# Performance work log

Hardware: AMD Instinct MI355X
Metric: run time of the kernel (lower is better)

## Reference

```python
import jax, jax.numpy as jnp
import numpy as np

N, E, G = 40000, 400000, 64
IN, ED, HID, HEADS, OUT = 2, 18, 64, 4, 3

def _glorot(key, shape):
    fan_in = shape[0]
    return jax.random.normal(key, shape, dtype=jnp.float32) / np.float32(np.sqrt(fan_in))

def setup_inputs():
    key = jax.random.key(0)
    ks = jax.random.split(key, 32)
    d1 = HEADS * HID  # 256
    return {
        "x": jax.random.normal(ks[0], (N, IN), jnp.float32),
        "edge_index": jax.random.randint(ks[1], (2, E), 0, N),
        "edge_attr": jax.random.normal(ks[2], (E, ED), jnp.float32),
        "batch": jnp.sort(jax.random.randint(ks[3], (N,), 0, G)),
        # conv1: TransformerConv(2 -> 64, heads=4, concat=True, beta=True, edge_dim=18)
        "Wq1": _glorot(ks[4], (IN, d1)), "bq1": jnp.zeros((d1,), jnp.float32),
        "Wk1": _glorot(ks[5], (IN, d1)), "bk1": jnp.zeros((d1,), jnp.float32),
        "Wv1": _glorot(ks[6], (IN, d1)), "bv1": jnp.zeros((d1,), jnp.float32),
        "We1": _glorot(ks[7], (ED, d1)),
        "Wskip1": _glorot(ks[8], (IN, d1)), "bskip1": jnp.zeros((d1,), jnp.float32),
        "Wbeta1": _glorot(ks[9], (3 * d1, 1)),
        # conv2: TransformerConv(256 -> 64, heads=1, concat=False, beta=True, edge_dim=18)
        "Wq2": _glorot(ks[10], (d1, HID)), "bq2": jnp.zeros((HID,), jnp.float32),
        "Wk2": _glorot(ks[11], (d1, HID)), "bk2": jnp.zeros((HID,), jnp.float32),
        "Wv2": _glorot(ks[12], (d1, HID)), "bv2": jnp.zeros((HID,), jnp.float32),
        "We2": _glorot(ks[13], (ED, HID)),
        "Wskip2": _glorot(ks[14], (d1, HID)), "bskip2": jnp.zeros((HID,), jnp.float32),
        "Wbeta2": _glorot(ks[15], (3 * HID, 1)),
        "Wlin": _glorot(ks[16], (HID, OUT)), "blin": jnp.zeros((OUT,), jnp.float32),
    }

def _tconv(x, src, dst, edge_attr, Wq, bq, Wk, bk, Wv, bv, We, Wskip, bskip, Wbeta, H, C, concat):
    # PyG TransformerConv with edge_dim, beta=True, root_weight=True (eval: dropout off)
    n = x.shape[0]
    q = (x @ Wq + bq).reshape(n, H, C)
    k = (x @ Wk + bk).reshape(n, H, C)
    v = (x @ Wv + bv).reshape(n, H, C)
    e = (edge_attr @ We).reshape(-1, H, C)              # [E,H,C]
    kj = k[src] + e                                      # key_j + edge
    alpha = jnp.einsum('ehc,ehc->eh', q[dst], kj) * (1.0 / (C ** 0.5))  # [E,H]
    # segment softmax over destination nodes
    amax = jax.ops.segment_max(alpha, dst, num_segments=n)
    ex = jnp.exp(alpha - amax[dst])
    den = jax.ops.segment_sum(ex, dst, num_segments=n)
    w = ex / (den[dst] + 1e-16)
    msg = (v[src] + e) * w[:, :, None]                   # [E,H,C]
    out = jax.ops.segment_sum(msg, dst, num_segments=n)  # [N,H,C]
    out = out.reshape(n, H * C) if concat else out.mean(axis=1)
    # beta-gated skip connection
    xr = x @ Wskip + bskip
    beta = jax.nn.sigmoid(jnp.concatenate([out, xr, out - xr], axis=-1) @ Wbeta)
    return beta * xr + (1.0 - beta) * out

def reference(x, edge_index, edge_attr, batch, Wq1, bq1, Wk1, bk1, Wv1, bv1, We1, Wskip1, bskip1, Wbeta1, Wq2, bq2, Wk2, bk2, Wv2, bv2, We2, Wskip2, bskip2, Wbeta2, Wlin, blin):
    src, dst = edge_index[0], edge_index[1]
    h = jax.nn.relu(_tconv(x, src, dst, edge_attr, Wq1, bq1, Wk1, bk1, Wv1, bv1, We1, Wskip1, bskip1, Wbeta1, HEADS, HID, True))
    h = jax.nn.relu(_tconv(h, src, dst, edge_attr, Wq2, bq2, Wk2, bk2, Wv2, bv2, We2, Wskip2, bskip2, Wbeta2, 1, HID, False))
    # global mean pool per graph
    s = jax.ops.segment_sum(h, batch, num_segments=G)
    cnt = jax.ops.segment_sum(jnp.ones((h.shape[0], 1), h.dtype), batch, num_segments=G)
    pooled = s / jnp.maximum(cnt, 1.0)
    return pooled @ Wlin + blin
```

## Files before the change

### kernel.cpp

```cpp
#include <hip/hip_runtime.h>
#include <hip/hip_fp16.h>

#define N_NODES 40000
#define N_EDGES 400000
#define N_GRAPHS 64
#define D1 256
#define HIDC 64
#define NHEADS 4
#define EDIM 18
#define EPAD 20
#define OUTF 3
#define APAD 264
#define NROWS2 32

typedef _Float16 f16x8 __attribute__((ext_vector_type(8)));
typedef float f32x4 __attribute__((ext_vector_type(4)));

__global__ void prep_w(const float* __restrict__ Wq, const float* __restrict__ bq,
                       const float* __restrict__ Wk, const float* __restrict__ bk,
                       const float* __restrict__ Wv, const float* __restrict__ bv,
                       const float* __restrict__ Ws, const float* __restrict__ bs,
                       const float* __restrict__ We2,
                       const float* __restrict__ Wq1, const float* __restrict__ bq1,
                       const float* __restrict__ Wk1, const float* __restrict__ bk1,
                       const float* __restrict__ We1,
                       __half* __restrict__ Bt, float* __restrict__ bias,
                       float* __restrict__ cbuf) {
    int c = blockIdx.x, k = threadIdx.x;
    if (c < 256) {
        int m = c >> 6, d = c & 63;
        const float* W = (m == 0) ? Wq : (m == 1) ? Wk : (m == 2) ? Wv : Ws;
        Bt[c * 256 + k] = __float2half(W[k * 64 + d]);
        if (k == 0) {
            const float* b = (m == 0) ? bq : (m == 1) ? bk : (m == 2) ? bv : bs;
            bias[c] = b[d];
        }
    } else if (c < 288) {
        int j = c - 256;
        float s = 0.f;
        if (j < EDIM)
            for (int cc = 0; cc < 64; ++cc) s += Wq[k * 64 + cc] * We2[j * 64 + cc];
        Bt[c * 256 + k] = __float2half(s);
        if (k == 0) {
            float b = 0.f;
            if (j < EDIM)
                for (int cc = 0; cc < 64; ++cc) b += bq[cc] * We2[j * 64 + cc];
            bias[c] = b;
        }
    } else {
        int t = k;
        if (t < 36) {
            int h = t / 9, r = t % 9, a = r / 3, b = r % 3;
            const float* A = (a == 0) ? Wq1 : (a == 1) ? Wq1 + D1 : bq1;
            const float* B = (b == 0) ? Wk1 : (b == 1) ? Wk1 + D1 : bk1;
            float s = 0.f;
            for (int cc = 0; cc < 64; ++cc) s += A[h * 64 + cc] * B[h * 64 + cc];
            cbuf[h * 63 + a * 3 + b] = s;
        } else if (t < 252) {
            int i = t - 36;
            int h = i / 54, rr = (i % 54) / 18, j = i % 18;
            const float* A = (rr == 0) ? Wq1 : (rr == 1) ? Wq1 + D1 : bq1;
            float s = 0.f;
            for (int cc = 0; cc < 64; ++cc) s += A[h * 64 + cc] * We1[j * D1 + h * 64 + cc];
            cbuf[h * 63 + 9 + rr * 18 + j] = s;
        }
    }
}

__global__ void initA(float* __restrict__ acc1, float* __restrict__ acc2,
                      float* __restrict__ out2, int* __restrict__ deg,
                      float* __restrict__ pooled,
                      int* __restrict__ gs, int* __restrict__ ge) {
    int t = blockIdx.x * 256 + threadIdx.x;
    acc1[t] = 0.f;
    if (t < N_NODES * 64) out2[t] = 0.f;
    if (t < N_NODES * 20) acc2[t] = 0.f;
    if (t < N_NODES) deg[t] = 0;
    if (t < N_GRAPHS * HIDC) pooled[t] = 0.f;
    if (t < N_GRAPHS) { gs[t] = 0; ge[t] = 0; }
}

__global__ void hist_kernel(const int* __restrict__ ei, int* __restrict__ deg,
                            const int* __restrict__ batch, int* __restrict__ gs,
                            int* __restrict__ ge) {
    int e = blockIdx.x * 256 + threadIdx.x;
    if (e < N_EDGES) atomicAdd(&deg[ei[N_EDGES + e]], 1);
    int n = e;
    if (n < N_NODES) {
        int b = batch[n];
        if (n == 0) gs[b] = 0;
        else { int pb = batch[n - 1]; if (pb != b) { ge[pb] = n; gs[b] = n; } }
        if (n == N_NODES - 1) ge[b] = N_NODES;
    }
}

__global__ void scanA(const int* __restrict__ deg, int* __restrict__ bsum) {
    __shared__ int s[256];
    int b = blockIdx.x, t = threadIdx.x;
    s[t] = (t < 160) ? deg[b * 160 + t] : 0;
    __syncthreads();
    for (int off = 128; off; off >>= 1) {
        if (t < off) s[t] += s[t + off];
        __syncthreads();
    }
    if (t == 0) bsum[b] = s[0];
}

__global__ void scanB(const int* __restrict__ bsum, int* __restrict__ boff) {
    __shared__ int s[256];
    int t = threadIdx.x;
    int v = (t < 250) ? bsum[t] : 0;
    s[t] = v;
    __syncthreads();
    for (int off = 1; off < 256; off <<= 1) {
        int add = (t >= off) ? s[t - off] : 0;
        __syncthreads();
        s[t] += add;
        __syncthreads();
    }
    if (t < 250) boff[t] = s[t] - v;
}

__global__ void scanC(const int* __restrict__ deg, const int* __restrict__ boff,
                      int* __restrict__ cursor) {
    __shared__ int s[256];
    int b = blockIdx.x, t = threadIdx.x;
    int v = (t < 160) ? deg[b * 160 + t] : 0;
    s[t] = v;
    __syncthreads();
    for (int off = 1; off < 256; off <<= 1) {
        int add = (t >= off) ? s[t - off] : 0;
        __syncthreads();
        s[t] += add;
        __syncthreads();
    }
    if (t < 160) cursor[b * 160 + t] = boff[b] + s[t] - v;
}

__global__ void scatterE(const int* __restrict__ ei, const float* __restrict__ ea,
                         const float* __restrict__ x, int* __restrict__ cursor,
                         int* __restrict__ src_s, int* __restrict__ dst_s,
                         float* __restrict__ ea_s) {
    int e = blockIdx.x * 256 + threadIdx.x;
    if (e >= N_EDGES) return;
    int src = ei[e], dst = ei[N_EDGES + e];
    const float2* sr = (const float2*)(ea + (size_t)e * EDIM);
    float2 s0 = sr[0], s1 = sr[1], s2 = sr[2], s3 = sr[3], s4 = sr[4],
           s5 = sr[5], s6 = sr[6], s7 = sr[7], s8 = sr[8];
    float2 xv = *(const float2*)(x + (size_t)src * 2);
    int p = atomicAdd(&cursor[dst], 1);
    src_s[p] = src;
    dst_s[p] = dst;
    float4* drow = (float4*)(ea_s + (size_t)p * EPAD);
    drow[0] = make_float4(s0.x, s0.y, s1.x, s1.y);
    drow[1] = make_float4(s2.x, s2.y, s3.x, s3.y);
    drow[2] = make_float4(s4.x, s4.y, s5.x, s5.y);
    drow[3] = make_float4(s6.x, s6.y, s7.x, s7.y);
    drow[4] = make_float4(s8.x, s8.y, xv.x, xv.y);
}

__global__ void logits1(const int* __restrict__ dst_s, const float* __restrict__ ea_s,
                        const float* __restrict__ x, const float* __restrict__ cbuf,
                        float* __restrict__ w1) {
    __shared__ float cb[252];
    int t = threadIdx.x;
    if (t < 252) cb[t] = cbuf[t];
    __syncthreads();
    int p = blockIdx.x * 256 + t;
    if (p >= N_EDGES) return;
    const float4* row = (const float4*)(ea_s + (size_t)p * EPAD);
    float4 r0 = row[0], r1 = row[1], r2 = row[2], r3 = row[3], r4 = row[4];
    float s[EDIM];
    s[0]=r0.x; s[1]=r0.y; s[2]=r0.z; s[3]=r0.w;
    s[4]=r1.x; s[5]=r1.y; s[6]=r1.z; s[7]=r1.w;
    s[8]=r2.x; s[9]=r2.y; s[10]=r2.z; s[11]=r2.w;
    s[12]=r3.x; s[13]=r3.y; s[14]=r3.z; s[15]=r3.w;
    s[16]=r4.x; s[17]=r4.y;
    float xs0 = r4.z, xs1 = r4.w;
    int dst = dst_s[p];
    float2 xd = *(const float2*)(x + (size_t)dst * 2);
    float w[NHEADS];
    #pragma unroll
    for (int h = 0; h < NHEADS; ++h) {
        const float* c = cb + h * 63;
        float alpha = 0.f;
        #pragma unroll
        for (int a = 0; a < 3; ++a) {
            float tv = c[a * 3] * xs0 + c[a * 3 + 1] * xs1 + c[a * 3 + 2];
            const float* cc = c + 9 + a * 18;
            #pragma unroll
            for (int j = 0; j < EDIM; ++j) tv += cc[j] * s[j];
            alpha += tv * ((a == 0) ? xd.x : (a == 1) ? xd.y : 1.f);
        }
        w[h] = __expf(alpha * 0.125f);
    }
    *(float4*)(w1 + (size_t)p * 4) = make_float4(w[0], w[1], w[2], w[3]);
}

__global__ void strip1f(const int* __restrict__ dst_s, const float* __restrict__ ea_s,
                        const float* __restrict__ w1, float* __restrict__ acc1) {
    int t = threadIdx.x;
    int strip = blockIdx.x * 2 + (t >> 7);
    int l = t & 127;
    int h = l >> 5, comp = l & 31;
    bool active = comp < 21;
    int voff = (comp == 0) ? 18 : (comp == 1) ? 19 : (comp >= 3 ? comp - 3 : 0);
    bool isone = (comp == 2);
    int cidx = h * 21 + comp;
    int p0 = strip * 16;
    int dsts[16]; float v[16]; float w[16];
    #pragma unroll
    for (int j = 0; j < 16; ++j) dsts[j] = dst_s[p0 + j];
    #pragma unroll
    for (int j = 0; j < 16; ++j) w[j] = w1[(size_t)(p0 + j) * 4 + h];
    #pragma unroll
    for (int j = 0; j < 16; ++j)
        v[j] = active ? (isone ? 1.f : ea_s[(size_t)(p0 + j) * EPAD + voff]) : 0.f;
    float acc = 0.f;
    int prev = dsts[0];
    #pragma unroll
    for (int j = 0; j < 16; ++j) {
        if (dsts[j] != prev) {
            if (active) atomicAdd(&acc1[(size_t)prev * 84 + cidx], acc);
            acc = 0.f; prev = dsts[j];
        }
        acc += w[j] * v[j];
    }
    if (active) atomicAdd(&acc1[(size_t)prev * 84 + cidx], acc);
}

__global__ void finalize1x(const float* __restrict__ x, const float* __restrict__ acc1,
                           const float* __restrict__ Wv, const float* __restrict__ bv,
                           const float* __restrict__ We, const float* __restrict__ Wskip,
                           const float* __restrict__ bskip, const float* __restrict__ Wbeta,
                           __half* __restrict__ h1f) {
    __shared__ float red[4][4];
    int nb = blockIdx.x * 4;
    int t = threadIdx.x;
    int h = t >> 6;
    float wv0 = Wv[t], wv1 = Wv[D1 + t], bvv = bv[t];
    float we[EDIM];
    #pragma unroll
    for (int j = 0; j < EDIM; ++j) we[j] = We[j * D1 + t];
    float ws0 = Wskip[t], ws1 = Wskip[D1 + t], bsv = bskip[t];
    float wb0 = Wbeta[t], wb1 = Wbeta[D1 + t], wb2 = Wbeta[2 * D1 + t];
    float o[4], xr[4], part[4];
    #pragma unroll
    for (int i = 0; i < 4; ++i) {
        int node = nb + i;
        const float* a = acc1 + (size_t)node * 84 + h * 21;
        float l = a[2];
        float oo = a[0] * wv0 + a[1] * wv1 + l * bvv;
        #pragma unroll
        for (int j = 0; j < EDIM; ++j) oo += a[3 + j] * we[j];
        oo /= (l + 1e-16f);
        float x0 = x[node * 2], x1 = x[node * 2 + 1];
        xr[i] = x0 * ws0 + x1 * ws1 + bsv;
        o[i] = oo;
        part[i] = oo * wb0 + xr[i] * wb1 + (oo - xr[i]) * wb2;
    }
    #pragma unroll
    for (int off = 32; off; off >>= 1) {
        #pragma unroll
        for (int i = 0; i < 4; ++i) part[i] += __shfl_xor(part[i], off);
    }
    if ((t & 63) == 0) {
        #pragma unroll
        for (int i = 0; i < 4; ++i) red[h][i] = part[i];
    }
    __syncthreads();
    #pragma unroll
    for (int i = 0; i < 4; ++i) {
        float tot = red[0][i] + red[1][i] + red[2][i] + red[3][i];
        float beta = 1.f / (1.f + __expf(-tot));
        h1f[(size_t)(nb + i) * D1 + t] =
            __float2half(fmaxf(beta * xr[i] + (1.f - beta) * o[i], 0.f));
    }
}

__device__ __forceinline__ void nl2_store(int c, int gr, float v,
        float* __restrict__ q2, float* __restrict__ k2, __half* __restrict__ v2h,
        float* __restrict__ xr2, float* __restrict__ qe) {
    if (c < 256) {
        int m = c >> 6, d = c & 63;
        if (m == 0)      q2[(size_t)gr * 64 + d] = v;
        else if (m == 1) k2[(size_t)gr * 64 + d] = v;
        else if (m == 2) v2h[(size_t)gr * 64 + d] = __float2half(v);
        else             xr2[(size_t)gr * 64 + d] = v;
    } else {
        qe[(size_t)gr * 32 + (c - 256)] = v;
    }
}

__global__ __launch_bounds__(256) void nl2_mfma(
        const __half* __restrict__ h1f, const __half* __restrict__ Bt,
        const float* __restrict__ bias,
        float* __restrict__ q2, float* __restrict__ k2,
        __half* __restrict__ v2h, float* __restrict__ xr2,
        float* __restrict__ qe) {
    __shared__ _Float16 As[NROWS2 * APAD];
    int t = threadIdx.x;
    int row0 = blockIdx.x * NROWS2;
    const float4* gsrc = (const float4*)(h1f + (size_t)row0 * 256);
    #pragma unroll
    for (int i = 0; i < NROWS2 / 8; ++i) {
        int li = i * 256 + t;
        int r = li >> 5, c8 = li & 31;
        *(float4*)(As + r * APAD + c8 * 8) = gsrc[li];
    }
    __syncthreads();
    int wave = t >> 6, lane = t & 63, quad = lane >> 4, mm = lane & 15;
    const _Float16* Bp = (const _Float16*)Bt;
    for (int ct = wave; ct < 18; ct += 4) {
        int c0 = ct * 16 + mm;
        const _Float16* b0 = Bp + (size_t)c0 * 256 + quad * 8;
        f16x8 b[8];
        #pragma unroll
        for (int s = 0; s < 8; ++s) b[s] = *(const f16x8*)(b0 + s * 32);
        float bz = bias[c0];
        #pragma unroll
        for (int rt = 0; rt < NROWS2 / 16; ++rt) {
            const _Float16* arow = As + (rt * 16 + mm) * APAD + quad * 8;
            f16x8 a[8];
            #pragma unroll
            for (int s = 0; s < 8; ++s) a[s] = *(const f16x8*)(arow + s * 32);
            f32x4 accA = {bz, bz, bz, bz};
            f32x4 accB = {0.f, 0.f, 0.f, 0.f};
            #pragma unroll
            for (int s = 0; s < 4; ++s) {
                accA = __builtin_amdgcn_mfma_f32_16x16x32_f16(a[s],     b[s],     accA, 0, 0, 0);
                accB = __builtin_amdgcn_mfma_f32_16x16x32_f16(a[s + 4], b[s + 4], accB, 0, 0, 0);
            }
            #pragma unroll
            for (int r = 0; r < 4; ++r) {
                int gr = row0 + rt * 16 + quad * 4 + r;
                nl2_store(c0, gr, accA[r] + accB[r], q2, k2, v2h, xr2, qe);
            }
        }
    }
}

#define LG2_BLOCKS 2048
#define LG2_WAVES (LG2_BLOCKS * 4)
__global__ void logits2(const int* __restrict__ src_s, const int* __restrict__ dst_s,
                        const float* __restrict__ ea_s, const float* __restrict__ q2,
                        const float* __restrict__ k2, const float* __restrict__ qe,
                        float* __restrict__ alpha2) {
    int t = threadIdx.x, wid = t >> 6, lane = t & 63;
    int w = blockIdx.x * 4 + wid;
    for (int base = w; base < N_EDGES; base += 2 * LG2_WAVES) {
        int p1 = base, p2 = base + LG2_WAVES;
        bool has2 = p2 < N_EDGES;
        int p2c = has2 ? p2 : p1;
        int s1 = src_s[p1], d1 = dst_s[p1];
        int s2 = src_s[p2c], d2 = dst_s[p2c];
        float dd1 = q2[(size_t)d1 * 64 + lane] * k2[(size_t)s1 * 64 + lane];
        float dd2 = q2[(size_t)d2 * 64 + lane] * k2[(size_t)s2 * 64 + lane];
        if (lane < 20) {
            dd1 += qe[(size_t)d1 * 32 + lane] * ea_s[(size_t)p1 * EPAD + lane];
            dd2 += qe[(size_t)d2 * 32 + lane] * ea_s[(size_t)p2c * EPAD + lane];
        }
        #pragma unroll
        for (int off = 32; off; off >>= 1) {
            dd1 += __shfl_xor(dd1, off);
            dd2 += __shfl_xor(dd2, off);
        }
        if (lane == 0) {
            alpha2[p1] = __expf(dd1 * 0.125f);
            if (has2) alpha2[p2] = __expf(dd2 * 0.125f);
        }
    }
}

__global__ void spmm2s(const int* __restrict__ dst_s, const int* __restrict__ src_s,
                       const float* __restrict__ alpha2, const __half* __restrict__ v2h,
                       const float* __restrict__ ea_s,
                       float* __restrict__ out2, float* __restrict__ acc2) {
    int t = threadIdx.x;
    int strip = blockIdx.x * 4 + (t >> 6);
    int lane = t & 63;
    int p0 = strip * 16;
    int dsts[16]; int srcs[16]; float w[16];
    #pragma unroll
    for (int j = 0; j < 16; ++j) dsts[j] = dst_s[p0 + j];
    #pragma unroll
    for (int j = 0; j < 16; ++j) srcs[j] = src_s[p0 + j];
    #pragma unroll
    for (int j = 0; j < 16; ++j) w[j] = alpha2[p0 + j];
    float vv[16]; float ev[16];
    #pragma unroll
    for (int j = 0; j < 16; ++j) vv[j] = __half2float(v2h[(size_t)srcs[j] * 64 + lane]);
    #pragma unroll
    for (int j = 0; j < 16; ++j)
        ev[j] = (lane < EDIM) ? ea_s[(size_t)(p0 + j) * EPAD + lane] : 1.f;
    float acc = 0.f, accS = 0.f;
    int prev = dsts[0];
    #pragma unroll
    for (int j = 0; j < 16; ++j) {
        if (dsts[j] != prev) {
            atomicAdd(&out2[(size_t)prev * 64 + lane], acc);
            if (lane < 19) atomicAdd(&acc2[(size_t)prev * 20 + lane], accS);
            acc = 0.f; accS = 0.f; prev = dsts[j];
        }
        acc += w[j] * vv[j];
        accS += w[j] * ev[j];
    }
    atomicAdd(&out2[(size_t)prev * 64 + lane], acc);
    if (lane < 19) atomicAdd(&acc2[(size_t)prev * 20 + lane], accS);
}

__global__ void finalize2x(const float* __restrict__ out2, const float* __restrict__ acc2,
                           const float* __restrict__ xr2, const float* __restrict__ We2,
                           const float* __restrict__ Wb2, float* __restrict__ h2) {
    __shared__ float w2s[EDIM * 64];
    int t = threadIdx.x;
    for (int i = t; i < EDIM * 64; i += 256) w2s[i] = We2[i];
    __syncthreads();
    int node = blockIdx.x * 4 + (t >> 6);
    int lane = t & 63;
    const float* a2 = acc2 + (size_t)node * 20;
    float num = out2[(size_t)node * 64 + lane];
    #pragma unroll
    for (int j = 0; j < EDIM; ++j) num += a2[j] * w2s[j * 64 + lane];
    float o = num / (a2[18] + 1e-16f);
    float xr = xr2[(size_t)node * 64 + lane];
    float part = o * Wb2[lane] + xr * Wb2[64 + lane] + (o - xr) * Wb2[128 + lane];
    #pragma unroll
    for (int off = 32; off; off >>= 1) part += __shfl_xor(part, off);
    float beta = 1.f / (1.f + __expf(-part));
    h2[(size_t)node * 64 + lane] = fmaxf(beta * xr + (1.f - beta) * o, 0.f);
}

__global__ void pool_kernel(const float* __restrict__ h2, const int* __restrict__ gs,
                            const int* __restrict__ ge, float* __restrict__ pooled) {
    __shared__ float red[4][64];
    int g = blockIdx.x >> 2, q = blockIdx.x & 3;
    int t = threadIdx.x, wv = t >> 6, lane = t & 63;
    int s = gs[g], e = ge[g];
    float sum = 0.f;
    for (int n = s + q * 4 + wv; n < e; n += 16) sum += h2[(size_t)n * 64 + lane];
    red[wv][lane] = sum;
    __syncthreads();
    if (wv == 0) {
        float v = red[0][lane] + red[1][lane] + red[2][lane] + red[3][lane];
        atomicAdd(&pooled[g * 64 + lane], v);
    }
}

__global__ void final_lin(const float* __restrict__ pooled, const int* __restrict__ gs,
                          const int* __restrict__ ge,
                          const float* __restrict__ Wlin, const float* __restrict__ blin,
                          float* __restrict__ out) {
    int t = threadIdx.x;
    if (t >= N_GRAPHS * OUTF) return;
    int g = t / OUTF, o = t % OUTF;
    int c = ge[g] - gs[g];
    float inv = 1.f / fmaxf((float)c, 1.f);
    float acc = 0.f;
    for (int kk = 0; kk < HIDC; ++kk) acc += pooled[g * 64 + kk] * Wlin[kk * OUTF + o];
    out[t] = acc * inv + blin[o];
}

extern "C" void kernel_launch(void* const* d_in, const int* in_sizes, int n_in,
                              void* d_out, int out_size, void* d_ws, size_t ws_size,
                              hipStream_t stream) {
    const float* x      = (const float*)d_in[0];
    const int*   ei     = (const int*)d_in[1];
    const float* ea     = (const float*)d_in[2];
    const int*   batch  = (const int*)d_in[3];
    const float* Wq1    = (const float*)d_in[4];  const float* bq1    = (const float*)d_in[5];
    const float* Wk1    = (const float*)d_in[6];  const float* bk1    = (const float*)d_in[7];
    const float* Wv1    = (const float*)d_in[8];  const float* bv1    = (const float*)d_in[9];
    const float* We1    = (const float*)d_in[10];
    const float* Wskip1 = (const float*)d_in[11]; const float* bskip1 = (const float*)d_in[12];
    const float* Wbeta1 = (const float*)d_in[13];
    const float* Wq2    = (const float*)d_in[14]; const float* bq2    = (const float*)d_in[15];
    const float* Wk2    = (const float*)d_in[16]; const float* bk2    = (const float*)d_in[17];
    const float* Wv2    = (const float*)d_in[18]; const float* bv2    = (const float*)d_in[19];
    const float* We2    = (const float*)d_in[20];
    const float* Wskip2 = (const float*)d_in[21]; const float* bskip2 = (const float*)d_in[22];
    const float* Wbeta2 = (const float*)d_in[23];
    const float* Wlin   = (const float*)d_in[24]; const float* blin   = (const float*)d_in[25];

    float* ptr = (float*)d_ws;
    float* q2     = ptr; ptr += (size_t)N_NODES * 64;
    float* k2     = ptr; ptr += (size_t)N_NODES * 64;
    float* xr2    = ptr; ptr += (size_t)N_NODES * 64;
    float* qe     = ptr; ptr += (size_t)N_NODES * 32;
    __half* v2h   = (__half*)ptr; ptr += (size_t)N_NODES * 32;
    float* ea_s   = ptr; ptr += (size_t)N_EDGES * EPAD;
    float* alpha2 = ptr; ptr += N_EDGES;
    float* acc2   = ptr; ptr += (size_t)N_NODES * 20;
    float* out2   = ptr; ptr += (size_t)N_NODES * 64;
    float* pooled = ptr; ptr += N_GRAPHS * HIDC;
    int*   gs     = (int*)ptr; ptr += N_GRAPHS;
    int*   ge     = (int*)ptr; ptr += N_GRAPHS;
    float* cbuf   = ptr; ptr += 256;
    float* bias   = ptr; ptr += 320;
    __half* Bt    = (__half*)ptr; ptr += (288 * 256) / 2;
    int*   src_s  = (int*)ptr; ptr += N_EDGES;
    int*   dst_s  = (int*)ptr; ptr += N_EDGES;
    int*   deg    = (int*)ptr; ptr += N_NODES;
    int*   cursor = (int*)ptr; ptr += N_NODES;
    int*   bsum   = (int*)ptr; ptr += 256;
    int*   boff   = (int*)ptr; ptr += 256;
    float* w1     = ptr; ptr += (size_t)N_EDGES * 4;
    float* h2     = ptr; ptr += (size_t)N_NODES * 84;
    float* acc1   = ptr; ptr += (size_t)N_NODES * 84;
    __half* h1f   = (__half*)ptr; ptr += (size_t)N_NODES * 128;

    const int EB = (N_EDGES + 255) / 256;

    prep_w<<<289, 256, 0, stream>>>(Wq2, bq2, Wk2, bk2, Wv2, bv2, Wskip2, bskip2, We2,
                                    Wq1, bq1, Wk1, bk1, We1, Bt, bias, cbuf);
    initA<<<(N_NODES * 84) / 256, 256, 0, stream>>>(acc1, acc2, out2, deg, pooled, gs, ge);
    hist_kernel<<<EB, 256, 0, stream>>>(ei, deg, batch, gs, ge);
    scanA<<<250, 256, 0, stream>>>(deg, bsum);
    scanB<<<1, 256, 0, stream>>>(bsum, boff);
    scanC<<<250, 256, 0, stream>>>(deg, boff, cursor);
    scatterE<<<EB, 256, 0, stream>>>(ei, ea, x, cursor, src_s, dst_s, ea_s);

    logits1<<<EB, 256, 0, stream>>>(dst_s, ea_s, x, cbuf, w1);
    strip1f<<<(N_EDGES / 16) / 2, 256, 0, stream>>>(dst_s, ea_s, w1, acc1);
    finalize1x<<<N_NODES / 4, 256, 0, stream>>>(x, acc1, Wv1, bv1, We1, Wskip1, bskip1,
                                                Wbeta1, h1f);

    nl2_mfma<<<N_NODES / NROWS2, 256, 0, stream>>>(h1f, Bt, bias, q2, k2, v2h, xr2, qe);
    logits2<<<LG2_BLOCKS, 256, 0, stream>>>(src_s, dst_s, ea_s, q2, k2, qe, alpha2);
    spmm2s<<<(N_EDGES / 16) / 4, 256, 0, stream>>>(dst_s, src_s, alpha2, v2h, ea_s,
                                                   out2, acc2);
    finalize2x<<<N_NODES / 4, 256, 0, stream>>>(out2, acc2, xr2, We2, Wbeta2, h2);

    pool_kernel<<<N_GRAPHS * 4, 256, 0, stream>>>(h2, gs, ge, pooled);
    final_lin<<<1, 256, 0, stream>>>(pooled, gs, ge, Wlin, blin, (float*)d_out);
}
```

Baseline: 396.2 us.

## Recast layer-1 finalize as fp16 MFMA GEMM with folded beta projection

Replaces the scalar per-node finalize for conv1 with a normalization pass (scale1) that writes fp16 per-head aggregates, followed by an MFMA GEMM against a precomputed block-diagonal weight matrix built from Wv1, bv1 and We1. The beta-gate logit is folded algebraically into an extra GEMM column plus three scalar bias terms precomputed in prep_w, which removes the cross-wave shuffle reduction. This trades an extra kernel launch and an fp16 intermediate buffer, with some precision loss in the aggregates, for matrix-core throughput and fewer redundant per-thread weight loads.

```diff
diff --git a/kernel.cpp b/kernel.cpp
--- a/kernel.cpp
+++ b/kernel.cpp
@@ -12,6 +12,7 @@
 #define OUTF 3
 #define APAD 264
 #define NROWS2 32
+#define AP1 104
 
 typedef _Float16 f16x8 __attribute__((ext_vector_type(8)));
 typedef float f32x4 __attribute__((ext_vector_type(4)));
@@ -24,8 +25,11 @@
                        const float* __restrict__ Wq1, const float* __restrict__ bq1,
                        const float* __restrict__ Wk1, const float* __restrict__ bk1,
                        const float* __restrict__ We1,
+                       const float* __restrict__ Wv1, const float* __restrict__ bv1,
+                       const float* __restrict__ Ws1, const float* __restrict__ bs1,
+                       const float* __restrict__ Wb1,
                        __half* __restrict__ Bt, float* __restrict__ bias,
-                       float* __restrict__ cbuf) {
+                       float* __restrict__ cbuf, __half* __restrict__ Btf) {
     int c = blockIdx.x, k = threadIdx.x;
     if (c < 256) {
         int m = c >> 6, d = c & 63;
@@ -47,7 +51,7 @@
                 for (int cc = 0; cc < 64; ++cc) b += bq[cc] * We2[j * 64 + cc];
             bias[c] = b;
         }
-    } else {
+    } else if (c == 288) {
         int t = k;
         if (t < 36) {
             int h = t / 9, r = t % 9, a = r / 3, b = r % 3;
@@ -63,6 +67,41 @@
             float s = 0.f;
             for (int cc = 0; cc < 64; ++cc) s += A[h * 64 + cc] * We1[j * D1 + h * 64 + cc];
             cbuf[h * 63 + 9 + rr * 18 + j] = s;
+        }
+    } else if (c < 561) {
+        int c2 = c - 289;
+        if (k < 96) {
+            int hk = k / 24, j = k % 24;
+            float val = 0.f;
+            if (c2 < 256) {
+                int hh = c2 >> 6;
+                if (hk == hh && j < 21) {
+                    val = (j == 0) ? Wv1[c2] : (j == 1) ? Wv1[D1 + c2] :
+                          (j == 2) ? bv1[c2] : We1[(j - 3) * D1 + c2];
+                }
+            } else if (c2 == 256) {
+                if (j < 21) {
+                    float s = 0.f;
+                    for (int d = 0; d < 64; ++d) {
+                        int col = hk * 64 + d;
+                        float wr = (j == 0) ? Wv1[col] : (j == 1) ? Wv1[D1 + col] :
+                                   (j == 2) ? bv1[col] : We1[(j - 3) * D1 + col];
+                        s += wr * (Wb1[col] + Wb1[2 * D1 + col]);
+                    }
+                    val = s;
+                }
+            }
+            Btf[c2 * 96 + k] = __float2half(val);
+        }
+    } else {
+        if (k < 3) {
+            float s = 0.f;
+            for (int d = 0; d < D1; ++d) {
+                float u = Wb1[D1 + d] - Wb1[2 * D1 + d];
+                float w = (k == 0) ? Ws1[d] : (k == 1) ? Ws1[D1 + d] : bs1[d];
+                s += w * u;
+            }
+            bias[288 + k] = s;
         }
     }
 }
@@ -229,52 +268,115 @@
     if (active) atomicAdd(&acc1[(size_t)prev * 84 + cidx], acc);
 }
 
-__global__ void finalize1x(const float* __restrict__ x, const float* __restrict__ acc1,
-                           const float* __restrict__ Wv, const float* __restrict__ bv,
-                           const float* __restrict__ We, const float* __restrict__ Wskip,
-                           const float* __restrict__ bskip, const float* __restrict__ Wbeta,
-                           __half* __restrict__ h1f) {
-    __shared__ float red[4][4];
-    int nb = blockIdx.x * 4;
-    int t = threadIdx.x;
-    int h = t >> 6;
-    float wv0 = Wv[t], wv1 = Wv[D1 + t], bvv = bv[t];
-    float we[EDIM];
-    #pragma unroll
-    for (int j = 0; j < EDIM; ++j) we[j] = We[j * D1 + t];
-    float ws0 = Wskip[t], ws1 = Wskip[D1 + t], bsv = bskip[t];
-    float wb0 = Wbeta[t], wb1 = Wbeta[D1 + t], wb2 = Wbeta[2 * D1 + t];
-    float o[4], xr[4], part[4];
-    #pragma unroll
-    for (int i = 0; i < 4; ++i) {
-        int node = nb + i;
+__global__ void scale1(const float* __restrict__ acc1, __half* __restrict__ ah) {
+    int tg = blockIdx.x * 256 + threadIdx.x;
+    int node = tg / 96, k = tg % 96;
+    int h = k / 24, j = k % 24;
+    float val = 0.f;
+    if (j < 21) {
         const float* a = acc1 + (size_t)node * 84 + h * 21;
         float l = a[2];
-        float oo = a[0] * wv0 + a[1] * wv1 + l * bvv;
+        float inv = 1.f / (l + 1e-16f);
+        val = (j == 2) ? l * inv : a[j] * inv;
+    }
+    ah[tg] = __float2half(val);
+}
+
+__global__ __launch_bounds__(256) void fin1_mfma(
+        const __half* __restrict__ ah, const __half* __restrict__ Btf,
+        const float* __restrict__ x, const float* __restrict__ bias,
+        const float* __restrict__ Wskip, const float* __restrict__ bskip,
+        __half* __restrict__ h1f) {
+    __shared__ _Float16 As[32 * AP1];
+    __shared__ float betaL[32];
+    int t = threadIdx.x;
+    int row0 = blockIdx.x * 32;
+    const float4* gsrc = (const float4*)(ah + (size_t)row0 * 96);
+    #pragma unroll
+    for (int i = 0; i < 2; ++i) {
+        int li = i * 256 + t;
+        if (li < 384) {
+            int r = li / 12, c8 = li % 12;
+            *(float4*)(As + r * AP1 + c8 * 8) = gsrc[li];
+        }
+    }
+    __syncthreads();
+    int wave = t >> 6, lane = t & 63, quad = lane >> 4, mm = lane & 15;
+    const _Float16* Bp = (const _Float16*)Btf;
+    int ct0 = (wave == 0) ? 16 : wave;
+    f32x4 st[2];
+    {
+        int c0 = ct0 * 16 + mm;
+        const _Float16* b0 = Bp + (size_t)c0 * 96 + quad * 8;
+        f16x8 b0v = *(const f16x8*)(b0);
+        f16x8 b1v = *(const f16x8*)(b0 + 32);
+        f16x8 b2v = *(const f16x8*)(b0 + 64);
         #pragma unroll
-        for (int j = 0; j < EDIM; ++j) oo += a[3 + j] * we[j];
-        oo /= (l + 1e-16f);
-        float x0 = x[node * 2], x1 = x[node * 2 + 1];
-        xr[i] = x0 * ws0 + x1 * ws1 + bsv;
-        o[i] = oo;
-        part[i] = oo * wb0 + xr[i] * wb1 + (oo - xr[i]) * wb2;
-    }
-    #pragma unroll
-    for (int off = 32; off; off >>= 1) {
+        for (int rt = 0; rt < 2; ++rt) {
+            const _Float16* ar = As + (rt * 16 + mm) * AP1 + quad * 8;
+            f32x4 acc = {0.f, 0.f, 0.f, 0.f};
+            acc = __builtin_amdgcn_mfma_f32_16x16x32_f16(*(const f16x8*)(ar),      b0v, acc, 0, 0, 0);
+            acc = __builtin_amdgcn_mfma_f32_16x16x32_f16(*(const f16x8*)(ar + 32), b1v, acc, 0, 0, 0);
+            acc = __builtin_amdgcn_mfma_f32_16x16x32_f16(*(const f16x8*)(ar + 64), b2v, acc, 0, 0, 0);
+            st[rt] = acc;
+        }
+        if (wave == 0 && mm == 0) {
+            #pragma unroll
+            for (int rt = 0; rt < 2; ++rt)
+                #pragma unroll
+                for (int r = 0; r < 4; ++r)
+                    betaL[rt * 16 + quad * 4 + r] = st[rt][r];
+        }
+    }
+    __syncthreads();
+    if (t < 32) {
+        int nd = row0 + t;
+        float x0 = x[nd * 2], x1 = x[nd * 2 + 1];
+        float lg = betaL[t] + x0 * bias[288] + x1 * bias[289] + bias[290];
+        betaL[t] = 1.f / (1.f + __expf(-lg));
+    }
+    __syncthreads();
+    if (wave != 0) {
+        int c0 = ct0 * 16 + mm;
+        float w0 = Wskip[c0], w1s = Wskip[D1 + c0], bsv = bskip[c0];
         #pragma unroll
-        for (int i = 0; i < 4; ++i) part[i] += __shfl_xor(part[i], off);
-    }
-    if ((t & 63) == 0) {
+        for (int rt = 0; rt < 2; ++rt)
+            #pragma unroll
+            for (int r = 0; r < 4; ++r) {
+                int lr = rt * 16 + quad * 4 + r, gr = row0 + lr;
+                float beta = betaL[lr];
+                float x0 = x[gr * 2], x1 = x[gr * 2 + 1];
+                float xr = x0 * w0 + x1 * w1s + bsv;
+                h1f[(size_t)gr * D1 + c0] =
+                    __float2half(fmaxf(beta * xr + (1.f - beta) * st[rt][r], 0.f));
+            }
+    }
+    int nit = (wave == 0) ? 5 : 4;
+    for (int it = 1; it < nit; ++it) {
+        int ct = (wave == 0) ? (it - 1) * 4 : wave + it * 4;
+        int c0 = ct * 16 + mm;
+        const _Float16* b0 = Bp + (size_t)c0 * 96 + quad * 8;
+        f16x8 b0v = *(const f16x8*)(b0);
+        f16x8 b1v = *(const f16x8*)(b0 + 32);
+        f16x8 b2v = *(const f16x8*)(b0 + 64);
+        float w0 = Wskip[c0], w1s = Wskip[D1 + c0], bsv = bskip[c0];
         #pragma unroll
-        for (int i = 0; i < 4; ++i) red[h][i] = part[i];
-    }
-    __syncthreads();
-    #pragma unroll
-    for (int i = 0; i < 4; ++i) {
-        float tot = red[0][i] + red[1][i] + red[2][i] + red[3][i];
-        float beta = 1.f / (1.f + __expf(-tot));
-        h1f[(size_t)(nb + i) * D1 + t] =
-            __float2half(fmaxf(beta * xr[i] + (1.f - beta) * o[i], 0.f));
+        for (int rt = 0; rt < 2; ++rt) {
+            const _Float16* ar = As + (rt * 16 + mm) * AP1 + quad * 8;
+            f32x4 acc = {0.f, 0.f, 0.f, 0.f};
+            acc = __builtin_amdgcn_mfma_f32_16x16x32_f16(*(const f16x8*)(ar),      b0v, acc, 0, 0, 0);
+            acc = __builtin_amdgcn_mfma_f32_16x16x32_f16(*(const f16x8*)(ar + 32), b1v, acc, 0, 0, 0);
+            acc = __builtin_amdgcn_mfma_f32_16x16x32_f16(*(const f16x8*)(ar + 64), b2v, acc, 0, 0, 0);
+            #pragma unroll
+            for (int r = 0; r < 4; ++r) {
+                int lr = rt * 16 + quad * 4 + r, gr = row0 + lr;
+                float beta = betaL[lr];
+                float x0 = x[gr * 2], x1 = x[gr * 2 + 1];
+                float xr = x0 * w0 + x1 * w1s + bsv;
+                h1f[(size_t)gr * D1 + c0] =
+                    __float2half(fmaxf(beta * xr + (1.f - beta) * acc[r], 0.f));
+            }
+        }
     }
 }
 
@@ -498,6 +600,8 @@
     float* cbuf   = ptr; ptr += 256;
     float* bias   = ptr; ptr += 320;
     __half* Bt    = (__half*)ptr; ptr += (288 * 256) / 2;
+    __half* Btf   = (__half*)ptr; ptr += (272 * 96) / 2;
+    __half* ah    = (__half*)ptr; ptr += (size_t)N_NODES * 48;
     int*   src_s  = (int*)ptr; ptr += N_EDGES;
     int*   dst_s  = (int*)ptr; ptr += N_EDGES;
     int*   deg    = (int*)ptr; ptr += N_NODES;
@@ -505,14 +609,16 @@
     int*   bsum   = (int*)ptr; ptr += 256;
     int*   boff   = (int*)ptr; ptr += 256;
     float* w1     = ptr; ptr += (size_t)N_EDGES * 4;
-    float* h2     = ptr; ptr += (size_t)N_NODES * 84;
+    float* h2     = ptr; ptr += (size_t)N_NODES * 64;
     float* acc1   = ptr; ptr += (size_t)N_NODES * 84;
     __half* h1f   = (__half*)ptr; ptr += (size_t)N_NODES * 128;
 
     const int EB = (N_EDGES + 255) / 256;
 
-    prep_w<<<289, 256, 0, stream>>>(Wq2, bq2, Wk2, bk2, Wv2, bv2, Wskip2, bskip2, We2,
-                                    Wq1, bq1, Wk1, bk1, We1, Bt, bias, cbuf);
+    prep_w<<<562, 256, 0, stream>>>(Wq2, bq2, Wk2, bk2, Wv2, bv2, Wskip2, bskip2, We2,
+                                    Wq1, bq1, Wk1, bk1, We1,
+                                    Wv1, bv1, Wskip1, bskip1, Wbeta1,
+                                    Bt, bias, cbuf, Btf);
     initA<<<(N_NODES * 84) / 256, 256, 0, stream>>>(acc1, acc2, out2, deg, pooled, gs, ge);
     hist_kernel<<<EB, 256, 0, stream>>>(ei, deg, batch, gs, ge);
     scanA<<<250, 256, 0, stream>>>(deg, bsum);
@@ -522,8 +628,8 @@
 
     logits1<<<EB, 256, 0, stream>>>(dst_s, ea_s, x, cbuf, w1);
     strip1f<<<(N_EDGES / 16) / 2, 256, 0, stream>>>(dst_s, ea_s, w1, acc1);
-    finalize1x<<<N_NODES / 4, 256, 0, stream>>>(x, acc1, Wv1, bv1, We1, Wskip1, bskip1,
-                                                Wbeta1, h1f);
+    scale1<<<(N_NODES * 96) / 256, 256, 0, stream>>>(acc1, ah);
+    fin1_mfma<<<N_NODES / 32, 256, 0, stream>>>(ah, Btf, x, bias, Wskip1, bskip1, h1f);
 
     nl2_mfma<<<N_NODES / NROWS2, 256, 0, stream>>>(h1f, Bt, bias, q2, k2, v2h, xr2, qe);
     logits2<<<LG2_BLOCKS, 256, 0, stream>>>(src_s, dst_s, ea_s, q2, k2, qe, alpha2);
```

Measured after the change: 400.6 us. About the same (+1.1%).
